# Kernel tuning notes

Hardware: AMD Instinct MI355X
Metric: run time of the kernel (lower is better)

The kernel has to match this reference:

```python
import math
import jax, jax.numpy as jnp
import numpy as np

D_MODEL = 512
N_HEADS = 8
FACTOR = 1
B, L = 16, 2048


def setup_inputs() -> dict:
    key = jax.random.key(0)
    ks = jax.random.split(key, 12)
    d = D_MODEL
    inp = {
        'queries': jax.random.normal(ks[0], (B, L, d), dtype=jnp.float32),
        'keys':    jax.random.normal(ks[1], (B, L, d), dtype=jnp.float32),
        'values':  jax.random.normal(ks[2], (B, L, d), dtype=jnp.float32),
        # projection params (nn.Linear: y = x @ W.T + b)
        'Wq': jax.random.normal(ks[3], (d, d), dtype=jnp.float32) * 0.02,
        'bq': jnp.zeros((d,), dtype=jnp.float32),
        'Wk': jax.random.normal(ks[4], (d, d), dtype=jnp.float32) * 0.02,
        'bk': jnp.zeros((d,), dtype=jnp.float32),
        'Wv': jax.random.normal(ks[5], (d, d), dtype=jnp.float32) * 0.02,
        'bv': jnp.zeros((d,), dtype=jnp.float32),
        'Wo': jax.random.normal(ks[6], (d, d), dtype=jnp.float32) * 0.02,
        'bo': jnp.zeros((d,), dtype=jnp.float32),
    }
    return inp


def _autocorrelation(q, k, v):
    # q, k, v: [B, H, E, L]
    length = q.shape[-1]
    q_fft = jnp.fft.rfft(q, axis=-1)
    k_fft = jnp.fft.rfft(k, axis=-1)
    corr = jnp.fft.irfft(q_fft * jnp.conj(k_fft), n=length, axis=-1)  # [B,H,E,L]

    # time_delay_agg_training
    top_k = int(FACTOR * math.log(length))  # static
    mean_value = corr.mean(axis=(1, 2))            # [B, L]
    _, index = jax.lax.top_k(mean_value.mean(axis=0), top_k)  # [k], batch-shared delays
    weights = mean_value[:, index]                 # [B, k]
    tmp_corr = jax.nn.softmax(weights, axis=-1)    # [B, k]

    # roll(values, -delay) == values[..., (arange(L)+delay) % L]
    idx = (jnp.arange(length)[None, :] + index[:, None]) % length  # [k, L]
    patterns = v[..., idx]                         # [B, H, E, k, L]
    delays_agg = jnp.einsum('bhekl,bk->bhel', patterns, tmp_corr)  # [B,H,E,L]
    return delays_agg


def reference(queries, keys, values, Wq, bq, Wk, bk, Wv, bv, Wo, bo):
    Bb, Ll, d = queries.shape
    H = N_HEADS
    E = d // H
    # projections, then [B, L, H, E] -> [B, H, E, L]
    q = (queries @ Wq.T + bq).reshape(Bb, Ll, H, E).transpose(0, 2, 3, 1)
    k = (keys    @ Wk.T + bk).reshape(Bb, Ll, H, E).transpose(0, 2, 3, 1)
    v = (values  @ Wv.T + bv).reshape(Bb, Ll, H, E).transpose(0, 2, 3, 1)

    agg = _autocorrelation(q, k, v)                 # [B, H, E, L]
    out = agg.transpose(0, 3, 1, 2).reshape(Bb, Ll, H * E)  # [B, L, d]
    return out @ Wo.T + bo
```

## Files before the change

### kernel.cpp

```cpp
#include <hip/hip_runtime.h>


typedef _Float16 f16;
typedef _Float16 f16x8 __attribute__((ext_vector_type(8)));
typedef _Float16 f16x4 __attribute__((ext_vector_type(4)));
typedef float    f32x4 __attribute__((ext_vector_type(4)));

#define PSI(i) ((i) + ((i) >> 3))
#define TWI(j) ((j) + ((j) >> 4))

__device__ __forceinline__ float2 f2add(float2 a, float2 b) { return make_float2(a.x + b.x, a.y + b.y); }
__device__ __forceinline__ float2 f2sub(float2 a, float2 b) { return make_float2(a.x - b.x, a.y - b.y); }
__device__ __forceinline__ float2 cmul(float2 a, float2 b)  { return make_float2(a.x * b.x - a.y * b.y, a.x * b.y + a.y * b.x); }

__global__ __launch_bounds__(256) void cvt_weights(
    const float* __restrict__ w0, const float* __restrict__ w1,
    const float* __restrict__ w2, const float* __restrict__ w3,
    f16* __restrict__ o0, f16* __restrict__ o1, f16* __restrict__ o2, f16* __restrict__ o3)
{
    const float* src = (blockIdx.y == 0) ? w0 : (blockIdx.y == 1) ? w1 : (blockIdx.y == 2) ? w2 : w3;
    f16*         dst = (blockIdx.y == 0) ? o0 : (blockIdx.y == 1) ? o1 : (blockIdx.y == 2) ? o2 : o3;
    const int i = blockIdx.x * 256 + threadIdx.x;
    float4 val = ((const float4*)src)[i];
    f16x4 h = { (f16)val.x, (f16)val.y, (f16)val.z, (f16)val.w };
    ((f16x4*)dst)[i] = h;
}

__device__ __forceinline__ void stage_f16(const f16* __restrict__ G, int row0, int k0,
                                          f16* __restrict__ lds, int tid)
{
#pragma unroll
    for (int q = 0; q < 4; ++q) {
        const int r = q * 64 + (tid >> 3);
        const int u = (tid & 7) ^ ((tid >> 3) & 7);
        const f16* g = G + (size_t)(row0 + r) * 512 + k0 + u * 8;
        f16* d = lds + q * 4096 + (tid >> 6) * 512;
        __builtin_amdgcn_global_load_lds(
            (const __attribute__((address_space(1))) void*)g,
            (__attribute__((address_space(3))) void*)d, 16, 0, 0);
    }
}

__device__ __forceinline__ void load_f32_slab(const float* __restrict__ G, int row0, int k0,
                                              int tid, float4* __restrict__ rg)
{
#pragma unroll
    for (int q = 0; q < 4; ++q) {
        const float* g = G + (size_t)(row0 + q * 64 + (tid >> 3)) * 512 + k0 + (tid & 7) * 8;
        rg[2 * q]     = *(const float4*)g;
        rg[2 * q + 1] = *(const float4*)(g + 4);
    }
}
__device__ __forceinline__ void write_f16_slab(f16* __restrict__ lds, int tid,
                                               const float4* __restrict__ rg)
{
#pragma unroll
    for (int q = 0; q < 4; ++q) {
        float4 a = rg[2 * q], b = rg[2 * q + 1];
        f16x8 h = { (f16)a.x, (f16)a.y, (f16)a.z, (f16)a.w,
                    (f16)b.x, (f16)b.y, (f16)b.z, (f16)b.w };
        const int uu = (tid & 7) ^ ((tid >> 3) & 7);
        *(f16x8*)(lds + q * 4096 + (tid >> 3) * 64 + (uu << 3)) = h;
    }
}

__device__ __forceinline__ void stage_agg(const f16* __restrict__ Vb_, int l0, int k0,
                                          const int* __restrict__ ssel, const float* __restrict__ sw,
                                          f16* __restrict__ lds, int tid)
{
    const f16* base = Vb_ + k0 + (tid & 7) * 8;
#pragma unroll
    for (int q = 0; q < 4; ++q) {
        const int l  = l0 + q * 64 + (tid >> 3);
        const int uu = (tid & 7) ^ ((tid >> 3) & 7);
        float a0 = 0.f, a1 = 0.f, a2 = 0.f, a3 = 0.f, a4 = 0.f, a5 = 0.f, a6 = 0.f, a7 = 0.f;
#pragma unroll
        for (int k = 0; k < 7; ++k) {
            const int lk = (l + ssel[k]) & 2047;
            f16x8 v = *(const f16x8*)(base + (size_t)lk * 512);
            const float w = sw[k];
            a0 += w * (float)v[0]; a1 += w * (float)v[1];
            a2 += w * (float)v[2]; a3 += w * (float)v[3];
            a4 += w * (float)v[4]; a5 += w * (float)v[5];
            a6 += w * (float)v[6]; a7 += w * (float)v[7];
        }
        f16x8 h = { (f16)a0, (f16)a1, (f16)a2, (f16)a3, (f16)a4, (f16)a5, (f16)a6, (f16)a7 };
        *(f16x8*)(lds + q * 4096 + (tid >> 3) * 64 + (uu << 3)) = h;
    }
}

template<int AF32, int BF32, int AGG, int F16OUT, int MT_L2, int NT_L2, int SWZ, int SPLITB>
__global__ __launch_bounds__(512, 2) void gemm_nt(
    const void* __restrict__ A0v, const void* __restrict__ B0v, const void* __restrict__ B1v,
    void* __restrict__ Cout, int N,
    const float* __restrict__ bias_q, const float* __restrict__ bias_k,
    const float* __restrict__ bias_col,
    const int* __restrict__ selp, const float* __restrict__ wsmp)
{
    constexpr int BM = 256, BN = 256, NKT = 8;
    constexpr int ESZ = F16OUT ? 2 : 4;

    __shared__ __align__(16) char smem[131072];
    f16* smA = (f16*)smem;
    f16* smB = (f16*)smem + 2 * BM * 64;

    const int tid  = threadIdx.x;
    const int wave = tid >> 6, lane = tid & 63;

    int mt, nt;
    if (SWZ == 1) {
        const int xcd = blockIdx.x & 7, slot = blockIdx.x >> 3;
        mt = slot & ((1 << MT_L2) - 1);
        nt = (xcd << (NT_L2 - 3)) | (slot >> MT_L2);
    } else if (SWZ == 2) {
        const int xcd = blockIdx.x & 7, slot = blockIdx.x >> 3;
        nt = slot & ((1 << NT_L2) - 1);
        mt = (xcd << (MT_L2 - 3)) | (slot >> NT_L2);
    } else {
        nt = blockIdx.x & ((1 << NT_L2) - 1);
        mt = blockIdx.x >> NT_L2;
    }
    const int m0 = mt * BM, n0 = nt * BN;

    const bool useB1 = SPLITB && (mt >= (1 << (MT_L2 - 1)));
    const void* Bgv = useB1 ? B1v : B0v;
    const float* brow = SPLITB
        ? (useB1 ? bias_k - (1 << (MT_L2 - 1)) * BM : bias_q)
        : bias_q;

    const f16*   Ah = (const f16*)A0v;
    const float* Af = (const float*)A0v;
    const f16*   Bh = (const f16*)Bgv;
    const float* Bf = (const float*)Bgv;

    int   ssel[7];
    float sw[7];
    const f16* Vbase = nullptr;
    int l0 = 0;
    if (AGG) {
        const int b = m0 >> 11;
        l0 = m0 & 2047;
        Vbase = Ah + (size_t)b * 2048 * 512;
#pragma unroll
        for (int k = 0; k < 7; ++k) { ssel[k] = selp[k]; sw[k] = wsmp[b * 7 + k]; }
    }

    f32x4 acc[8][4];
#pragma unroll
    for (int m = 0; m < 8; ++m)
#pragma unroll
        for (int n = 0; n < 4; ++n) acc[m][n] = (f32x4){0.f, 0.f, 0.f, 0.f};

    const int fr = lane & 15;
    const int kg = (lane >> 4) * 8;
    const int rowm = fr & 7;
    const int wr = wave >> 2;
    const int wc = wave & 3;
    const int warow = wr * 128 + fr;
    const int wbrow = wc * 64 + fr;

    auto compute = [&](const f16* __restrict__ Ab, const f16* __restrict__ Bb) {
#pragma unroll
        for (int k2 = 0; k2 < 2; ++k2) {
            const int kb = k2 * 32 + kg;
            const int col = ((kb >> 3) ^ rowm) << 3;
            f16x8 af[8], bf[4];
#pragma unroll
            for (int m = 0; m < 8; ++m) af[m] = *(const f16x8*)&Ab[(warow + m * 16) * 64 + col];
#pragma unroll
            for (int n = 0; n < 4; ++n) bf[n] = *(const f16x8*)&Bb[(wbrow + n * 16) * 64 + col];
#pragma unroll
            for (int m = 0; m < 8; ++m)
#pragma unroll
                for (int n = 0; n < 4; ++n)
                    acc[m][n] = __builtin_amdgcn_mfma_f32_16x16x32_f16(af[m], bf[n], acc[m][n], 0, 0, 0);
        }
    };

    float4 ra[8], rb[8];

    if (AGG)       stage_agg(Vbase, l0, 0, ssel, sw, smA, tid);
    else if (AF32) { load_f32_slab(Af, m0, 0, tid, ra); write_f16_slab(smA, tid, ra); }
    else           stage_f16(Ah, m0, 0, smA, tid);
    if (BF32) { load_f32_slab(Bf, n0, 0, tid, rb); write_f16_slab(smB, tid, rb); }
    else      stage_f16(Bh, n0, 0, smB, tid);
    asm volatile("s_waitcnt vmcnt(0) lgkmcnt(0)" ::: "memory");
    __builtin_amdgcn_s_barrier();

#pragma unroll 1
    for (int kk = 0; kk < NKT; ++kk) {
        const int cur = kk & 1;
        if (kk < NKT - 1) {
            const int k0 = (kk + 1) * 64;
            if (AGG)       stage_agg(Vbase, l0, k0, ssel, sw, smA + (cur ^ 1) * BM * 64, tid);
            else if (AF32) load_f32_slab(Af, m0, k0, tid, ra);
            else           stage_f16(Ah, m0, k0, smA + (cur ^ 1) * BM * 64, tid);
            if (BF32) load_f32_slab(Bf, n0, k0, tid, rb);
            else      stage_f16(Bh, n0, k0, smB + (cur ^ 1) * BN * 64, tid);
        }
        compute(smA + cur * BM * 64, smB + cur * BN * 64);
        if (kk < NKT - 1) {
            if (AF32) write_f16_slab(smA + (cur ^ 1) * BM * 64, tid, ra);
            if (BF32) write_f16_slab(smB + (cur ^ 1) * BN * 64, tid, rb);
        }
        asm volatile("s_waitcnt vmcnt(0) lgkmcnt(0)" ::: "memory");
        __builtin_amdgcn_s_barrier();
    }

    constexpr int L     = F16OUT ? 3 : 2;
    constexpr int CPR   = (BN * ESZ) / 16;
    constexpr int HROWS = F16OUT ? 256 : 128;
    constexpr int NH    = F16OUT ? 1 : 2;
#pragma unroll 1
    for (int h = 0; h < NH; ++h) {
        __syncthreads();
        if (F16OUT || wr == h) {
            const int lr0 = wr * 128 + ((lane >> 4) << 2);
#pragma unroll
            for (int m = 0; m < 8; ++m)
#pragma unroll
                for (int n = 0; n < 4; ++n) {
                    const int col = wc * 64 + n * 16 + fr;
                    const float bc = bias_col ? bias_col[n0 + col] : 0.f;
#pragma unroll
                    for (int j = 0; j < 4; ++j) {
                        const int row  = lr0 + m * 16 + j;
                        const int rl   = row - h * HROWS * (F16OUT ? 0 : 1);
                        const int scol = ((((col >> L) ^ (row & 7)) << L) | (col & ((1 << L) - 1)));
                        float v = acc[m][n][j] + bc + (brow ? brow[m0 + row] : 0.f);
                        if (F16OUT) ((f16*)smem)[row * BN + scol] = (f16)v;
                        else        ((float*)smem)[rl * BN + scol] = v;
                    }
                }
        }
        __syncthreads();
        const int chunks = HROWS * CPR;
#pragma unroll 1
        for (int i = tid; i < chunks; i += 512) {
            const int rl  = i / CPR;
            const int u   = i % CPR;
            const int row = h * HROWS + rl;
            int4 vv = *(const int4*)(smem + (rl * CPR + (u ^ (row & 7))) * 16);
            *(int4*)((char*)Cout + ((size_t)(m0 + row) * N + n0) * ESZ + u * 16) = vv;
        }
    }
}

template<int S>
__device__ __forceinline__ void fft_pass2(float2* __restrict__ z, const float2* __restrict__ tw, int tid)
{
    constexpr int m = 1024 >> S;
    constexpr int h = m >> 1;
#pragma unroll
    for (int rep = 0; rep < 2; ++rep) {
        const int idx = tid + rep * 256;
        const int j2  = idx & (h - 1);
        const int blk = idx >> (9 - S);
        const int i   = (blk << (11 - S)) + j2;
        const float2 w1 = tw[TWI(j2 << S)];
        const float2 w2 = tw[TWI(j2 << (S + 1))];
        float2 a = z[PSI(i)], b = z[PSI(i + h)], c = z[PSI(i + m)], d = z[PSI(i + m + h)];
        float2 a1 = f2add(a, c);
        float2 c1 = cmul(f2sub(a, c), w1);
        float2 b1 = f2add(b, d);
        float2 t0 = cmul(f2sub(b, d), w1);
        float2 d1 = make_float2(t0.y, -t0.x);
        z[PSI(i)]         = f2add(a1, b1);
        z[PSI(i + h)]     = cmul(f2sub(a1, b1), w2);
        z[PSI(i + m)]     = f2add(c1, d1);
        z[PSI(i + m + h)] = cmul(f2sub(c1, d1), w2);
    }
    __syncthreads();
}

__device__ __forceinline__ void fft_tail_scatter(float2* __restrict__ z, int tid)
{
    float2 v[8];
    const int p0 = tid * 8;
#pragma unroll
    for (int e = 0; e < 8; ++e) v[e] = z[PSI(p0 + e)];
    __syncthreads();
    constexpr float RS = 0.70710678118654752f;
    const float2 W8[4] = { {1.f, 0.f}, {RS, -RS}, {0.f, -1.f}, {-RS, -RS} };
#pragma unroll
    for (int e = 0; e < 4; ++e) {
        float2 t = f2sub(v[e], v[e + 4]);
        v[e]     = f2add(v[e], v[e + 4]);
        v[e + 4] = cmul(t, W8[e]);
    }
#pragma unroll
    for (int base = 0; base < 8; base += 4) {
        float2 t0 = f2sub(v[base], v[base + 2]);
        v[base]     = f2add(v[base], v[base + 2]);
        v[base + 2] = t0;
        float2 t1 = f2sub(v[base + 1], v[base + 3]);
        v[base + 1] = f2add(v[base + 1], v[base + 3]);
        v[base + 3] = make_float2(t1.y, -t1.x);
    }
#pragma unroll
    for (int base = 0; base < 8; base += 2) {
        float2 t = f2sub(v[base], v[base + 1]);
        v[base]     = f2add(v[base], v[base + 1]);
        v[base + 1] = t;
    }
    const int br8t = (int)(__brev((unsigned)tid) >> 24);
    const int BR3[8] = {0, 4, 2, 6, 1, 5, 3, 7};
#pragma unroll
    for (int e = 0; e < 8; ++e) {
        const int f = br8t + (BR3[e] << 8);
        z[PSI(f)] = v[e];
    }
    __syncthreads();
}

__device__ __forceinline__ void fft2048_natural(float2* __restrict__ z, const float2* __restrict__ tw, int tid)
{
    fft_pass2<0>(z, tw, tid);
    fft_pass2<2>(z, tw, tid);
    fft_pass2<4>(z, tw, tid);
    fft_pass2<6>(z, tw, tid);
    fft_tail_scatter(z, tid);
}

__device__ __forceinline__ void fill_tw(float2* __restrict__ tw, int tid)
{
    for (int j = tid; j < 1024; j += 256) {
        float sv, cv;
        sincospif(-(float)j * (1.0f / 1024.0f), &sv, &cv);
        tw[TWI(j)] = make_float2(cv, sv);
    }
}

__global__ __launch_bounds__(256) void fft_corr(
    const f16* __restrict__ Qt, const f16* __restrict__ Kt,
    float2* __restrict__ Sp)
{
    __shared__ float2 z[2304];
    __shared__ float2 tw[1088];
    const int tid = threadIdx.x;
    const int grp = blockIdx.x;
    const int b   = blockIdx.y;

    fill_tw(tw, tid);
    float2 racc[5];
#pragma unroll
    for (int r = 0; r < 5; ++r) racc[r] = make_float2(0.f, 0.f);
    __syncthreads();

    for (int ch = 0; ch < 4; ++ch) {
        const int c = grp * 4 + ch;
        const f16x8* qr = (const f16x8*)(Qt + ((size_t)c * 16 + b) * 2048);
        const f16x8* kr = (const f16x8*)(Kt + ((size_t)c * 16 + b) * 2048);
        f16x8 qv = qr[tid], kv = kr[tid];
        const int e0 = tid * 8;
#pragma unroll
        for (int j = 0; j < 8; ++j)
            z[PSI(e0 + j)] = make_float2((float)qv[j], (float)kv[j]);
        __syncthreads();
        fft2048_natural(z, tw, tid);
#pragma unroll
        for (int r = 0; r < 5; ++r) {
            const int f = tid + (r << 8);
            if (f <= 1024) {
                const int pf = (2048 - f) & 2047;
                float2 Zf  = z[PSI(f)];
                float2 Zc0 = z[PSI(pf)];
                float qx = 0.5f * (Zf.x + Zc0.x), qy = 0.5f * (Zf.y - Zc0.y);
                float dx = Zf.x - Zc0.x,          dy = Zf.y + Zc0.y;
                float kx = 0.5f * dy,             ky = -0.5f * dx;
                racc[r].x += qx * kx + qy * ky;
                racc[r].y += qy * kx - qx * ky;
            }
        }
        __syncthreads();
    }
    float2* out = Sp + ((size_t)b * 128 + grp) * 1025;
#pragma unroll
    for (int r = 0; r < 5; ++r) {
        const int f = tid + (r << 8);
        if (f <= 1024) out[f] = racc[r];
    }
}

__global__ __launch_bounds__(256) void reduce_sp(
    const float2* __restrict__ Sp, float2* __restrict__ Sred)
{
    const int b = blockIdx.x;
    const int f = blockIdx.y * 256 + threadIdx.x;
    if (f > 1024) return;
    const float2* base = Sp + (size_t)b * 128 * 1025 + f;
    float sx = 0.f, sy = 0.f;
#pragma unroll 8
    for (int g = 0; g < 128; ++g) {
        float2 p = base[(size_t)g * 1025];
        sx += p.x; sy += p.y;
    }
    Sred[b * 1025 + f] = make_float2(sx, sy);
}

__global__ __launch_bounds__(256) void ifft_mean(
    const float2* __restrict__ Sred, float* __restrict__ mv)
{
    __shared__ float2 z[2304];
    __shared__ float2 tw[1088];
    const int tid = threadIdx.x;
    const int b   = blockIdx.x;
    fill_tw(tw, tid);
#pragma unroll
    for (int r = 0; r < 5; ++r) {
        const int f = tid + (r << 8);
        if (f <= 1024) {
            float2 s = Sred[b * 1025 + f];
            z[PSI(f)] = make_float2(s.x, -s.y);
            if (f >= 1 && f <= 1023)
                z[PSI(2048 - f)] = make_float2(s.x, s.y);
        }
    }
    __syncthreads();
    fft2048_natural(z, tw, tid);
    const float scale = 1.0f / (2048.0f * 512.0f);
    for (int t = tid; t < 2048; t += 256)
        mv[(size_t)b * 2048 + t] = z[PSI(t)].x * scale;
}

__global__ __launch_bounds__(256) void select_topk(
    const float* __restrict__ mv, int* __restrict__ sel, float* __restrict__ wsm)
{
    __shared__ float u[2048];
    __shared__ float rv[256];
    __shared__ int   ri[256];
    __shared__ int   ssel[7];
    const int tid = threadIdx.x;
    for (int t = tid; t < 2048; t += 256) {
        float s = 0.f;
        for (int b = 0; b < 16; ++b) s += mv[b * 2048 + t];
        u[t] = s;
    }
    __syncthreads();
    for (int k = 0; k < 7; ++k) {
        float best = -3.4e38f; int bi = 0x7fffffff;
        for (int t = tid; t < 2048; t += 256)
            if (u[t] > best) { best = u[t]; bi = t; }
        rv[tid] = best; ri[tid] = bi;
        __syncthreads();
        for (int off = 128; off > 0; off >>= 1) {
            if (tid < off) {
                if (rv[tid + off] > rv[tid] ||
                    (rv[tid + off] == rv[tid] && ri[tid + off] < ri[tid])) {
                    rv[tid] = rv[tid + off]; ri[tid] = ri[tid + off];
                }
            }
            __syncthreads();
        }
        if (tid == 0) { ssel[k] = ri[0]; sel[k] = ri[0]; u[ri[0]] = -3.4e38f; }
        __syncthreads();
    }
    if (tid < 16) {
        float vals[7], mx = -3.4e38f;
        for (int k = 0; k < 7; ++k) { vals[k] = mv[tid * 2048 + ssel[k]]; mx = fmaxf(mx, vals[k]); }
        float se = 0.f;
        for (int k = 0; k < 7; ++k) { vals[k] = expf(vals[k] - mx); se += vals[k]; }
        for (int k = 0; k < 7; ++k) wsm[tid * 7 + k] = vals[k] / se;
    }
}

extern "C" void kernel_launch(void* const* d_in, const int* in_sizes, int n_in,
                              void* d_out, int out_size, void* d_ws, size_t ws_size,
                              hipStream_t stream)
{
    (void)in_sizes; (void)n_in; (void)out_size; (void)ws_size;
    const float* queries = (const float*)d_in[0];
    const float* keys    = (const float*)d_in[1];
    const float* values  = (const float*)d_in[2];
    const float* Wq = (const float*)d_in[3];
    const float* bq = (const float*)d_in[4];
    const float* Wk = (const float*)d_in[5];
    const float* bk = (const float*)d_in[6];
    const float* Wv = (const float*)d_in[7];
    const float* bv = (const float*)d_in[8];
    const float* Wo = (const float*)d_in[9];
    const float* bo = (const float*)d_in[10];

    char* p = (char*)d_ws;
    f16*    QKt = (f16*)p;    p += 67108864;
    f16*    Vb  = (f16*)p;    p += 33554432;
    f16*    wqh = (f16*)p;    p += 524288;
    f16*    wkh = (f16*)p;    p += 524288;
    f16*    wvh = (f16*)p;    p += 524288;
    f16*    woh = (f16*)p;    p += 524288;
    float2* Sp  = (float2*)p; p += 16793600;
    float2* Srd = (float2*)p; p += 131200;
    float*  mv  = (float*)p;  p += 131072;
    int*    sel = (int*)p;    p += 256;
    float*  wsm = (float*)p;  p += 512;
    f16*    Kt  = QKt + (size_t)512 * 32768;

    cvt_weights<<<dim3(256, 4), 256, 0, stream>>>(Wq, Wk, Wv, Wo, wqh, wkh, wvh, woh);

    gemm_nt<0, 1, 0, 1, 2, 7, 1, 1><<<512, 512, 0, stream>>>(
        wqh, queries, keys, QKt, 32768, bq, bk, nullptr, nullptr, nullptr);

    gemm_nt<1, 0, 0, 1, 7, 1, 2, 0><<<256, 512, 0, stream>>>(
        values, wvh, nullptr, Vb, 512, nullptr, nullptr, bv, nullptr, nullptr);

    fft_corr<<<dim3(128, 16), 256, 0, stream>>>(QKt, Kt, Sp);
    reduce_sp<<<dim3(16, 5), 256, 0, stream>>>(Sp, Srd);
    ifft_mean<<<16, 256, 0, stream>>>(Srd, mv);
    select_topk<<<1, 256, 0, stream>>>(mv, sel, wsm);

    gemm_nt<0, 0, 1, 0, 7, 1, 2, 0><<<256, 512, 0, stream>>>(
        Vb, woh, nullptr, (float*)d_out, 512, nullptr, nullptr, bo, sel, wsm);
}
```

Before: 264.9 us.

## Deepen fp32 operand prefetch to two stages with partial vmcnt waits

The GEMM main loop now keeps two register sets of fp32 operand slabs, so global loads for tile k+2 are issued while tile k computes and tile k+1 is written to shared memory. The wait before each barrier becomes a partial vmcnt(8) wait, so the newest loads stay in flight across the barrier. This aims to hide global-load latency for the fp32-input projections, at the cost of more registers (a second ra/rb set) and possibly lower occupancy. The loop is unrolled by two so the register sets alternate, and it assumes NKT is even.

After: 441.3 us. 1.67x slower.

```diff
diff --git a/kernel.cpp b/kernel.cpp
--- a/kernel.cpp
+++ b/kernel.cpp
@@ -177,35 +177,53 @@
         }
     };
 
-    float4 ra[8], rb[8];
-
-    if (AGG)       stage_agg(Vbase, l0, 0, ssel, sw, smA, tid);
-    else if (AF32) { load_f32_slab(Af, m0, 0, tid, ra); write_f16_slab(smA, tid, ra); }
-    else           stage_f16(Ah, m0, 0, smA, tid);
-    if (BF32) { load_f32_slab(Bf, n0, 0, tid, rb); write_f16_slab(smB, tid, rb); }
-    else      stage_f16(Bh, n0, 0, smB, tid);
-    asm volatile("s_waitcnt vmcnt(0) lgkmcnt(0)" ::: "memory");
+    float4 ra0[8], ra1[8], rb0[8], rb1[8];
+
+    if (BF32) load_f32_slab(Bf, n0, 0, tid, rb0);
+    if (AF32) load_f32_slab(Af, m0, 0, tid, ra0);
+    if (AGG)              stage_agg(Vbase, l0, 0, ssel, sw, smA, tid);
+    if (!AF32 && !AGG)    stage_f16(Ah, m0, 0, smA, tid);
+    if (!BF32)            stage_f16(Bh, n0, 0, smB, tid);
+    if (BF32) write_f16_slab(smB, tid, rb0);
+    if (AF32) write_f16_slab(smA, tid, ra0);
+    if (BF32) load_f32_slab(Bf, n0, 64, tid, rb1);
+    if (AF32) load_f32_slab(Af, m0, 64, tid, ra1);
+    if (AF32 || BF32) { asm volatile("s_waitcnt vmcnt(8) lgkmcnt(0)" ::: "memory"); }
+    else              { asm volatile("s_waitcnt vmcnt(0) lgkmcnt(0)" ::: "memory"); }
     __builtin_amdgcn_s_barrier();
 
+#define PIPE_BODY(KK, RB_W, RB_L, RA_W, RA_L)                                       \
+    {                                                                               \
+        const int kk_ = (KK);                                                       \
+        const int nb_ = (kk_ + 1) & 1;                                              \
+        if (kk_ + 1 < NKT) {                                                        \
+            if (BF32) write_f16_slab(smB + nb_ * BN * 64, tid, RB_W);               \
+            if (AF32) write_f16_slab(smA + nb_ * BM * 64, tid, RA_W);               \
+            if (AGG)  stage_agg(Vbase, l0, (kk_ + 1) * 64, ssel, sw,                \
+                                smA + nb_ * BM * 64, tid);                          \
+            if (!AF32 && !AGG) stage_f16(Ah, m0, (kk_ + 1) * 64,                    \
+                                         smA + nb_ * BM * 64, tid);                 \
+            if (!BF32) stage_f16(Bh, n0, (kk_ + 1) * 64, smB + nb_ * BN * 64, tid); \
+        }                                                                           \
+        if (kk_ + 2 < NKT) {                                                        \
+            if (BF32) load_f32_slab(Bf, n0, (kk_ + 2) * 64, tid, RB_L);             \
+            if (AF32) load_f32_slab(Af, m0, (kk_ + 2) * 64, tid, RA_L);             \
+        }                                                                           \
+        compute(smA + (kk_ & 1) * BM * 64, smB + (kk_ & 1) * BN * 64);              \
+        if ((kk_ + 2 < NKT) && (AF32 || BF32)) {                                    \
+            asm volatile("s_waitcnt vmcnt(8) lgkmcnt(0)" ::: "memory");             \
+        } else if (kk_ + 1 < NKT) {                                                 \
+            asm volatile("s_waitcnt vmcnt(0) lgkmcnt(0)" ::: "memory");             \
+        }                                                                           \
+        if (kk_ + 1 < NKT) __builtin_amdgcn_s_barrier();                            \
+    }
+
 #pragma unroll 1
-    for (int kk = 0; kk < NKT; ++kk) {
-        const int cur = kk & 1;
-        if (kk < NKT - 1) {
-            const int k0 = (kk + 1) * 64;
-            if (AGG)       stage_agg(Vbase, l0, k0, ssel, sw, smA + (cur ^ 1) * BM * 64, tid);
-            else if (AF32) load_f32_slab(Af, m0, k0, tid, ra);
-            else           stage_f16(Ah, m0, k0, smA + (cur ^ 1) * BM * 64, tid);
-            if (BF32) load_f32_slab(Bf, n0, k0, tid, rb);
-            else      stage_f16(Bh, n0, k0, smB + (cur ^ 1) * BN * 64, tid);
-        }
-        compute(smA + cur * BM * 64, smB + cur * BN * 64);
-        if (kk < NKT - 1) {
-            if (AF32) write_f16_slab(smA + (cur ^ 1) * BM * 64, tid, ra);
-            if (BF32) write_f16_slab(smB + (cur ^ 1) * BN * 64, tid, rb);
-        }
-        asm volatile("s_waitcnt vmcnt(0) lgkmcnt(0)" ::: "memory");
-        __builtin_amdgcn_s_barrier();
-    }
+    for (int kks = 0; kks < NKT; kks += 2) {
+        PIPE_BODY(kks,     rb1, rb0, ra1, ra0);
+        PIPE_BODY(kks + 1, rb0, rb1, ra0, ra1);
+    }
+#undef PIPE_BODY
 
     constexpr int L     = F16OUT ? 3 : 2;
     constexpr int CPR   = (BN * ESZ) / 16;
```

## Single-buffer GEMM shared memory to fit more workgroups per CU

Applied to the files above, without the earlier changes.

Halves the GEMM's LDS footprint by dropping double buffering of the A/B slabs and raises the launch-bounds occupancy hint from 2 to 4 blocks per CU. The main loop becomes stage, barrier, compute, barrier, so global loads no longer overlap MFMA work within a block. The epilogue now writes output through LDS in more, smaller chunks. The bet is that more resident blocks hide latency better than in-block prefetch did, at the risk of register spills (256 accumulator floats per thread under a tighter bound) and lost overlap.

New measurement: 790.8 us. +198.6%, slower.

```diff
diff --git a/kernel.cpp b/kernel.cpp
--- a/kernel.cpp
+++ b/kernel.cpp
@@ -90,7 +90,7 @@
 }
 
 template<int AF32, int BF32, int AGG, int F16OUT, int MT_L2, int NT_L2, int SWZ, int SPLITB>
-__global__ __launch_bounds__(512, 2) void gemm_nt(
+__global__ __launch_bounds__(512, 4) void gemm_nt(
     const void* __restrict__ A0v, const void* __restrict__ B0v, const void* __restrict__ B1v,
     void* __restrict__ Cout, int N,
     const float* __restrict__ bias_q, const float* __restrict__ bias_k,
@@ -100,9 +100,9 @@
     constexpr int BM = 256, BN = 256, NKT = 8;
     constexpr int ESZ = F16OUT ? 2 : 4;
 
-    __shared__ __align__(16) char smem[131072];
+    __shared__ __align__(16) char smem[65536];
     f16* smA = (f16*)smem;
-    f16* smB = (f16*)smem + 2 * BM * 64;
+    f16* smB = (f16*)smem + BM * 64;
 
     const int tid  = threadIdx.x;
     const int wave = tid >> 6, lane = tid & 63;
@@ -159,16 +159,27 @@
     const int warow = wr * 128 + fr;
     const int wbrow = wc * 64 + fr;
 
-    auto compute = [&](const f16* __restrict__ Ab, const f16* __restrict__ Bb) {
+    float4 ra[8], rb[8];
+
+    auto stage_slab = [&](int kk) {
+        const int k0 = kk * 64;
+        if (AGG)       stage_agg(Vbase, l0, k0, ssel, sw, smA, tid);
+        else if (AF32) { load_f32_slab(Af, m0, k0, tid, ra); write_f16_slab(smA, tid, ra); }
+        else           stage_f16(Ah, m0, k0, smA, tid);
+        if (BF32) { load_f32_slab(Bf, n0, k0, tid, rb); write_f16_slab(smB, tid, rb); }
+        else      stage_f16(Bh, n0, k0, smB, tid);
+    };
+
+    auto compute = [&]() {
 #pragma unroll
         for (int k2 = 0; k2 < 2; ++k2) {
             const int kb = k2 * 32 + kg;
             const int col = ((kb >> 3) ^ rowm) << 3;
             f16x8 af[8], bf[4];
 #pragma unroll
-            for (int m = 0; m < 8; ++m) af[m] = *(const f16x8*)&Ab[(warow + m * 16) * 64 + col];
-#pragma unroll
-            for (int n = 0; n < 4; ++n) bf[n] = *(const f16x8*)&Bb[(wbrow + n * 16) * 64 + col];
+            for (int m = 0; m < 8; ++m) af[m] = *(const f16x8*)&smA[(warow + m * 16) * 64 + col];
+#pragma unroll
+            for (int n = 0; n < 4; ++n) bf[n] = *(const f16x8*)&smB[(wbrow + n * 16) * 64 + col];
 #pragma unroll
             for (int m = 0; m < 8; ++m)
 #pragma unroll
@@ -177,64 +188,51 @@
         }
     };
 
-    float4 ra[8], rb[8];
-
-    if (AGG)       stage_agg(Vbase, l0, 0, ssel, sw, smA, tid);
-    else if (AF32) { load_f32_slab(Af, m0, 0, tid, ra); write_f16_slab(smA, tid, ra); }
-    else           stage_f16(Ah, m0, 0, smA, tid);
-    if (BF32) { load_f32_slab(Bf, n0, 0, tid, rb); write_f16_slab(smB, tid, rb); }
-    else      stage_f16(Bh, n0, 0, smB, tid);
-    asm volatile("s_waitcnt vmcnt(0) lgkmcnt(0)" ::: "memory");
-    __builtin_amdgcn_s_barrier();
-
+    stage_slab(0);
+    __syncthreads();
 #pragma unroll 1
     for (int kk = 0; kk < NKT; ++kk) {
-        const int cur = kk & 1;
-        if (kk < NKT - 1) {
-            const int k0 = (kk + 1) * 64;
-            if (AGG)       stage_agg(Vbase, l0, k0, ssel, sw, smA + (cur ^ 1) * BM * 64, tid);
-            else if (AF32) load_f32_slab(Af, m0, k0, tid, ra);
-            else           stage_f16(Ah, m0, k0, smA + (cur ^ 1) * BM * 64, tid);
-            if (BF32) load_f32_slab(Bf, n0, k0, tid, rb);
-            else      stage_f16(Bh, n0, k0, smB + (cur ^ 1) * BN * 64, tid);
-        }
-        compute(smA + cur * BM * 64, smB + cur * BN * 64);
-        if (kk < NKT - 1) {
-            if (AF32) write_f16_slab(smA + (cur ^ 1) * BM * 64, tid, ra);
-            if (BF32) write_f16_slab(smB + (cur ^ 1) * BN * 64, tid, rb);
-        }
-        asm volatile("s_waitcnt vmcnt(0) lgkmcnt(0)" ::: "memory");
-        __builtin_amdgcn_s_barrier();
+        compute();
+        if (kk + 1 < NKT) {
+            __syncthreads();
+            stage_slab(kk + 1);
+            __syncthreads();
+        }
     }
 
     constexpr int L     = F16OUT ? 3 : 2;
     constexpr int CPR   = (BN * ESZ) / 16;
-    constexpr int HROWS = F16OUT ? 256 : 128;
-    constexpr int NH    = F16OUT ? 1 : 2;
-#pragma unroll 1
+    constexpr int NH    = (BM * BN * ESZ) / 65536;
+    constexpr int HROWS = BM / NH;
+    constexpr int MPP   = HROWS / 16;
+#pragma unroll
     for (int h = 0; h < NH; ++h) {
         __syncthreads();
-        if (F16OUT || wr == h) {
-            const int lr0 = wr * 128 + ((lane >> 4) << 2);
-#pragma unroll
-            for (int m = 0; m < 8; ++m)
+        const int hw  = (h * HROWS) >> 7;
+        const int mlo = ((h * HROWS) & 127) >> 4;
+        if (wr == hw) {
+            const int r0 = (lane >> 4) << 2;
+#pragma unroll
+            for (int mm = 0; mm < MPP; ++mm) {
+                const int m = mlo + mm;
 #pragma unroll
                 for (int n = 0; n < 4; ++n) {
                     const int col = wc * 64 + n * 16 + fr;
                     const float bc = bias_col ? bias_col[n0 + col] : 0.f;
 #pragma unroll
                     for (int j = 0; j < 4; ++j) {
-                        const int row  = lr0 + m * 16 + j;
-                        const int rl   = row - h * HROWS * (F16OUT ? 0 : 1);
+                        const int row  = wr * 128 + r0 + m * 16 + j;
+                        const int rl   = row - h * HROWS;
                         const int scol = ((((col >> L) ^ (row & 7)) << L) | (col & ((1 << L) - 1)));
                         float v = acc[m][n][j] + bc + (brow ? brow[m0 + row] : 0.f);
-                        if (F16OUT) ((f16*)smem)[row * BN + scol] = (f16)v;
+                        if (F16OUT) ((f16*)smem)[rl * BN + scol] = (f16)v;
                         else        ((float*)smem)[rl * BN + scol] = v;
                     }
                 }
+            }
         }
         __syncthreads();
-        const int chunks = HROWS * CPR;
+        constexpr int chunks = HROWS * CPR;
 #pragma unroll 1
         for (int i = tid; i < chunks; i += 512) {
             const int rl  = i / CPR;
```
